# Kernel tuning notes

Measured on AMD Instinct MI355X. Metric: run time of the kernel, lower is better.

## Reference

```python
import jax, jax.numpy as jnp
import numpy as np

HEADS = 16
LN_EPS = 1e-5


def setup_inputs() -> dict:
    key = jax.random.key(0)
    ks = jax.random.split(key, 4)
    B, S, C, U = 2, 2048, 1024, 1024
    scale = 1.0 / np.sqrt(C)
    return {
        "inputs": jax.random.normal(ks[0], (B, S, C), dtype=jnp.float32),
        "Wq": jax.random.normal(ks[1], (C, U), dtype=jnp.float32) * scale,
        "bq": jnp.zeros((U,), dtype=jnp.float32),
        "Wk": jax.random.normal(ks[2], (C, U), dtype=jnp.float32) * scale,
        "bk": jnp.zeros((U,), dtype=jnp.float32),
        "Wv": jax.random.normal(ks[3], (C, U), dtype=jnp.float32) * scale,
        "bv": jnp.zeros((U,), dtype=jnp.float32),
        "ln_gamma": jnp.ones((S, U), dtype=jnp.float32),
        "ln_beta": jnp.zeros((S, U), dtype=jnp.float32),
    }


def reference(inputs, Wq, bq, Wk, bk, Wv, bv, ln_gamma, ln_beta):
    B, S, C = inputs.shape
    U = Wq.shape[1]
    H = HEADS
    dh = U // H

    Q = inputs @ Wq + bq  # [B,S,U]
    K = inputs @ Wk + bk
    V = inputs @ Wv + bv

    # torch: concat(split(X, U//H, dim=-1), dim=0) -> head-major stacking on batch
    def split_heads(X):
        return jnp.moveaxis(X.reshape(B, S, H, dh), 2, 0).reshape(H * B, S, dh)

    Q_, K_, V_ = split_heads(Q), split_heads(K), split_heads(V)

    scores = jnp.einsum('bqd,bkd->bqk', Q_, K_) / jnp.sqrt(jnp.float32(dh))
    tri = jnp.tril(jnp.ones((S, S), dtype=bool))  # causal mask
    scores = jnp.where(tri[None, :, :], scores, jnp.float32(-1e9))
    attn = jax.nn.softmax(scores, axis=-1)
    out_ = jnp.einsum('bqk,bkd->bqd', attn, V_)  # [H*B,S,dh]

    # inverse: split on batch into H chunks of size B, concat on feature dim
    out = jnp.moveaxis(out_.reshape(H, B, S, dh), 0, 2).reshape(B, S, U)

    out = out + inputs  # residual

    # LayerNorm over normalized_shape=[S, U] (joint seq+feature stats)
    mu = jnp.mean(out, axis=(-2, -1), keepdims=True)
    var = jnp.mean(jnp.square(out - mu), axis=(-2, -1), keepdims=True)
    out = (out - mu) / jnp.sqrt(var + LN_EPS) * ln_gamma + ln_beta
    return out
```

## Files before the change

kernel.cpp:

```cpp
#include <hip/hip_runtime.h>
#include <hip/hip_bf16.h>


typedef __bf16 bf16_t;
typedef __bf16 bf16x8 __attribute__((ext_vector_type(8)));
typedef __bf16 bf16x4 __attribute__((ext_vector_type(4)));
typedef _Float16 f16_t;
typedef _Float16 f16x2 __attribute__((ext_vector_type(2)));
typedef _Float16 f16x4 __attribute__((ext_vector_type(4)));
typedef _Float16 f16x8 __attribute__((ext_vector_type(8)));
typedef float f32x4 __attribute__((ext_vector_type(4)));

constexpr int Bsz = 2;
constexpr int Seq = 2048;
constexpr int Cdim = 1024;
constexpr int Udim = 1024;
constexpr int Hn = 16;
constexpr int Dh = 64;
constexpr int Mrows = Bsz * Seq;
constexpr int PerBatch = Seq * Udim;
constexpr float SCLQ = 0.125f * 1.44269504088896340736f;

#if __has_builtin(__builtin_amdgcn_exp2f)
#define EXP2F(x) __builtin_amdgcn_exp2f(x)
#else
#define EXP2F(x) exp2f(x)
#endif

#define AINL __attribute__((always_inline))
#define BARRIER() __builtin_amdgcn_s_barrier()
#define SCHEDB() __builtin_amdgcn_sched_barrier(0)
#define WAITV4() asm volatile("s_waitcnt vmcnt(4)" ::: "memory")
#define WAITV0() asm volatile("s_waitcnt vmcnt(0)" ::: "memory")

__device__ __forceinline__ void gload16(const void* g, void* l)
{
    __builtin_amdgcn_global_load_lds(
        (const __attribute__((address_space(1))) void*)g,
        (__attribute__((address_space(3))) void*)l, 16, 0, 0);
}

__device__ __forceinline__ f16x2 pkrtz(float a, float b)
{
    return __builtin_bit_cast(f16x2, __builtin_amdgcn_cvt_pkrtz(a, b));
}

__global__ __launch_bounds__(256)
void prep(const float* __restrict__ X,
          const float* __restrict__ Wq, const float* __restrict__ Wk,
          const float* __restrict__ Wv,
          bf16_t* __restrict__ Xb,
          bf16_t* __restrict__ Tq, bf16_t* __restrict__ Tk,
          bf16_t* __restrict__ Tv, float* __restrict__ stats)
{
    int z = blockIdx.z;
    int tid = threadIdx.x;
    if (z < 3) {
        const float* W = (z == 0) ? Wq : (z == 1) ? Wk : Wv;
        bf16_t* T = (z == 0) ? Tq : (z == 1) ? Tk : Tv;
        __shared__ bf16_t t[64][65];
        int x0 = blockIdx.x * 64, y0 = blockIdx.y * 64;
        int tx = tid & 63, ty = tid >> 6;
        for (int i = ty; i < 64; i += 4)
            t[i][tx] = (bf16_t)W[(size_t)(y0 + i) * Cdim + x0 + tx];
        __syncthreads();
        for (int i = ty; i < 64; i += 4)
            T[(size_t)(x0 + i) * Cdim + y0 + tx] = t[tx][i];
    } else {
        int bi = blockIdx.y * 16 + blockIdx.x;
        if (bi == 0 && tid < 4) stats[tid] = 0.0f;
        const float4* Xv = (const float4*)X;
#pragma unroll
        for (int k = 0; k < 16; k++) {
            int i = bi * 4096 + k * 256 + tid;
            float4 v = Xv[i];
            bf16x4 o = { (bf16_t)v.x, (bf16_t)v.y, (bf16_t)v.z, (bf16_t)v.w };
            *(bf16x4*)(Xb + (size_t)i * 4) = o;
        }
    }
}

__global__ __launch_bounds__(256)
void gemm_qkv(const bf16_t* __restrict__ X,
              const bf16_t* __restrict__ Wt0, const bf16_t* __restrict__ Wt1,
              const bf16_t* __restrict__ Wt2,
              const float* __restrict__ b0, const float* __restrict__ b1,
              const float* __restrict__ b2,
              f16_t* __restrict__ O0, f16_t* __restrict__ O1, f16_t* __restrict__ O2v)
{
    int z = blockIdx.z;
    const bf16_t* Wt = (z == 0) ? Wt0 : (z == 1) ? Wt1 : Wt2;
    const float* bias = (z == 0) ? b0 : (z == 1) ? b1 : b2;
    float scl = (z == 0) ? SCLQ : 1.0f;

    constexpr int Kd = 1024, Nd = 1024;
    __shared__ __align__(16) bf16_t As[2][4096];
    __shared__ __align__(16) bf16_t Bs[2][4096];

    int tid = threadIdx.x;
    int wave = tid >> 6, lane = tid & 63, quad = lane >> 4, l16 = lane & 15;
    int wm = (wave & 1) * 64, wn = (wave >> 1) * 64;
    int m0 = blockIdx.y * 128, n0 = blockIdx.x * 128;

    f32x4 acc[4][4] = {};

    int e0 = wave * 512 + lane * 8;
    int r0 = e0 >> 5, c0 = e0 & 31;
    int e1 = e0 + 2048;
    int r1 = e1 >> 5, c1 = e1 & 31;
    const bf16_t* Ag = X + (size_t)m0 * Kd;
    const bf16_t* Bg = Wt + (size_t)n0 * Kd;

    auto STG = [&](int nb, int k0) AINL {
        gload16(Ag + (size_t)r0 * Kd + k0 + c0, &As[nb][wave * 512]);
        gload16(Ag + (size_t)r1 * Kd + k0 + c1, &As[nb][2048 + wave * 512]);
        gload16(Bg + (size_t)r0 * Kd + k0 + c0, &Bs[nb][wave * 512]);
        gload16(Bg + (size_t)r1 * Kd + k0 + c1, &Bs[nb][2048 + wave * 512]);
    };

    int kNext = 32;
    auto STEP = [&](int buf, bool doStage) AINL {
        BARRIER();
        if (doStage) { STG(buf ^ 1, kNext); kNext += 32; WAITV4(); }
        else WAITV0();
        BARRIER();
        SCHEDB();
        bf16x8 af[4], bfr[4];
#pragma unroll
        for (int i = 0; i < 4; i++)
            af[i] = *(const bf16x8*)&As[buf][(wm + i * 16 + l16) * 32 + quad * 8];
#pragma unroll
        for (int i = 0; i < 4; i++)
            bfr[i] = *(const bf16x8*)&Bs[buf][(wn + i * 16 + l16) * 32 + quad * 8];
#pragma unroll
        for (int mt = 0; mt < 4; mt++)
#pragma unroll
            for (int nt = 0; nt < 4; nt++)
                acc[mt][nt] = __builtin_amdgcn_mfma_f32_16x16x32_bf16(
                    af[mt], bfr[nt], acc[mt][nt], 0, 0, 0);
    };

    STG(0, 0);
    for (int it = 0; it < 15; it++) { STEP(0, true); STEP(1, true); }
    STEP(0, true);
    STEP(1, false);

    if (z < 2) {
        f16_t* Og = (z == 0) ? O0 : O1;
#pragma unroll
        for (int nt = 0; nt < 4; nt++) {
            int col = n0 + wn + nt * 16 + l16;
            float bv = bias[col];
#pragma unroll
            for (int mt = 0; mt < 4; mt++) {
                int row = m0 + wm + mt * 16 + quad * 4;
#pragma unroll
                for (int r = 0; r < 4; r++)
                    Og[(size_t)(row + r) * Nd + col] = (f16_t)((acc[mt][nt][r] + bv) * scl);
            }
        }
    } else {
        int bb = m0 >> 11;
#pragma unroll
        for (int nt = 0; nt < 4; nt++) {
            int col = n0 + wn + nt * 16 + l16;
            float bv = bias[col];
            int h = col >> 6, d = col & 63;
            f16_t* vbase = O2v + (((size_t)(bb * Hn + h) * Dh + d) << 11);
#pragma unroll
            for (int mt = 0; mt < 4; mt++) {
                int row = m0 + wm + mt * 16 + quad * 4;
                int s = row & (Seq - 1);
                f16x4 pk;
#pragma unroll
                for (int r = 0; r < 4; r++) pk[r] = (f16_t)(acc[mt][nt][r] + bv);
                *(f16x4*)(vbase + s) = pk;
            }
        }
    }
}

__global__ __launch_bounds__(512, 4)
void attn15(const f16_t* __restrict__ Q, const f16_t* __restrict__ K,
            const f16_t* __restrict__ Vt, const float* __restrict__ X,
            bf16_t* __restrict__ R, float* __restrict__ stats)
{
    int id = blockIdx.x;
    int c = id & 7;
    int rr = id >> 3;
    int g = rr & 3;
    int pi = rr >> 2;
    int bh = (g << 3) | c;
    int b = bh >> 4, h = bh & 15;
    int qa = 31 - pi, qb = pi, split = 15 - pi;

    int tid = threadIdx.x;
    int grp = tid >> 8;
    int w = (tid >> 6) & 3;
    int lane = tid & 63, quad = lane >> 4, l16 = lane & 15;
    size_t bS = (size_t)b * Seq;

    __shared__ __align__(16) char ldsRaw[65600];
    f16_t* KsBase = (f16_t*)(ldsRaw + grp * 32768);
    f16_t* VsBase = (f16_t*)(ldsRaw + grp * 32768 + 16384);
    float* cmbO   = (float*)(ldsRaw + 32768);
    float* cmbLS  = (float*)(ldsRaw + 49152);
    float* red    = (float*)(ldsRaw + 65536);

    const f16_t* Kg = K + bS * Udim + h * Dh;
    const f16_t* Vg = Vt + ((size_t)(b * Hn + h)) * Dh * Seq;

    int srow = w * 8 + (lane >> 3);
    int schunk = (lane & 7) ^ ((lane >> 3) & 7);

    int qidxA = qa * 64 + w * 16 + l16;
    int qidxB = qb * 64 + w * 16 + l16;
    const f16_t* QpA = Q + (bS + qidxA) * Udim + h * Dh;
    const f16_t* QpB = Q + (bS + qidxB) * Udim + h * Dh;
    f16x8 qfA[2], qfB[2];
#pragma unroll
    for (int s2 = 0; s2 < 2; s2++) {
        qfA[s2] = *(const f16x8*)(QpA + s2 * 32 + quad * 8);
        qfB[s2] = *(const f16x8*)(QpB + s2 * 32 + quad * 8);
    }

    int m = l16 & 7;
    int kO0 = l16 * 64 + ((quad ^ m) << 3);
    int kO1 = l16 * 64 + (((4 + quad) ^ m) << 3);
    int vO[4];
#pragma unroll
    for (int t = 0; t < 4; t++)
        vO[t] = l16 * 64 + (((t * 32 + quad * 8) ^ (m << 4)) >> 1);

    f32x4 OA[4] = {}, OB[4] = {};
    float lsA = 0.0f, lsB = 0.0f;
    f32x4 stX[4], stY[4];

    auto tl0 = [&](int rho) AINL -> int { return (rho <= qb) ? rho : rho - qb - 1; };

    auto STAGE_K = [&](int nb, int tl) AINL {
        const f16_t* kp = Kg + (size_t)(tl * 64 + srow) * Udim + schunk * 8;
        f16_t* kd = KsBase + nb * 4096;
        gload16(kp, kd + w * 512);
        gload16(kp + (size_t)32 * Udim, kd + 2048 + w * 512);
    };
    auto STAGE_V = [&](int nb, int tl) AINL {
        const f16_t* vp = Vg + (size_t)srow * Seq + tl * 64 + schunk * 8;
        f16_t* vd = VsBase + nb * 4096;
        gload16(vp, vd + w * 512);
        gload16(vp + (size_t)32 * Seq, vd + 2048 + w * 512);
    };

    auto QK = [&](int buf, const f16x8 (&qf)[2], f32x4 (&sOUT)[4], int tcap) AINL {
        const f16_t* Kb = KsBase + buf * 4096;
#pragma unroll
        for (int t = 0; t < 4; t++) {
            if (t <= tcap) {
                f16x8 kf0 = *(const f16x8*)&Kb[kO0 + t * 1024];
                f16x8 kf1 = *(const f16x8*)&Kb[kO1 + t * 1024];
                f32x4 a = {};
                a = __builtin_amdgcn_mfma_f32_16x16x32_f16(kf0, qf[0], a, 0, 0, 0);
                a = __builtin_amdgcn_mfma_f32_16x16x32_f16(kf1, qf[1], a, 0, 0, 0);
                sOUT[t] = a;
            }
        }
    };

    auto SMPV = [&](f32x4 (&sIN)[4], f32x4 (&O)[4], float& ls, bool msk,
                    int kv0, int qidx, int tcap, int vbuf) AINL {
        const f16_t* Vb = VsBase + vbuf * 4096;
#pragma unroll
        for (int t = 0; t < 4; t++) {
            if (t <= tcap) {
                float pv[4];
#pragma unroll
                for (int r2 = 0; r2 < 4; r2++) {
                    float sv = sIN[t][r2];
                    if (msk && (kv0 + t * 16 + quad * 4 + r2 > qidx)) sv = -1e30f;
                    pv[r2] = EXP2F(sv);
                    ls += pv[r2];
                }
                f16x2 lo = pkrtz(pv[0], pv[1]);
                f16x2 hi = pkrtz(pv[2], pv[3]);
                f16x4 pf;
                pf[0] = lo[0]; pf[1] = lo[1]; pf[2] = hi[0]; pf[3] = hi[1];
#pragma unroll
                for (int dt = 0; dt < 4; dt++) {
                    f16x4 vf = *(const f16x4*)&Vb[vO[t] + dt * 1024];
                    O[dt] = __builtin_amdgcn_mfma_f32_16x16x16f16(vf, pf, O[dt], 0, 0, 0);
                }
            }
        }
    };

    auto ROUND = [&](int r, int buf, f32x4 (&sIN)[4], f32x4 (&sOUT)[4]) AINL {
        if (grp == 0) {
            if (r <= 14) STAGE_K(buf ^ 1, tl0(r + 1));
            if (r <= 15) STAGE_V(buf ^ 1, tl0(r));
        } else {
            if (r <= 15) STAGE_K(buf ^ 1, split + r + 1);
            STAGE_V(buf ^ 1, split + r);
        }
        if (grp == 0) {
            if (r <= 15) {
                if (r <= qb) QK(buf, qfB, sOUT, (r == qb) ? w : 3);
                else         QK(buf, qfA, sOUT, 3);
            }
        } else {
            QK(buf, qfA, sOUT, (r == 16) ? w : 3);
        }
        if (r >= 1) {
            if (grp == 0) {
                if (r <= qb)          SMPV(sIN, OB, lsB, false, 0, 0, 3, buf);
                else if (r == qb + 1) SMPV(sIN, OB, lsB, true, qb * 64, qidxB, w, buf);
                else                  SMPV(sIN, OA, lsA, false, 0, 0, 3, buf);
            } else {
                SMPV(sIN, OA, lsA, false, 0, 0, 3, buf);
            }
        }
        __syncthreads();
    };

    STAGE_K(0, (grp == 0) ? 0 : split);
    __syncthreads();

    for (int i = 0; i < 8; i++) {
        ROUND(2 * i, 0, stX, stY);
        ROUND(2 * i + 1, 1, stY, stX);
    }
    ROUND(16, 0, stX, stY);

    if (grp == 1)
        SMPV(stY, OA, lsA, true, qa * 64, qidxA, w, 1);

    __syncthreads();

    lsA += __shfl_xor(lsA, 16);
    lsA += __shfl_xor(lsA, 32);

    float s_acc = 0.0f, ss_acc = 0.0f;

    if (grp == 1) {
        float* po = cmbO + w * 1024 + lane * 16;
#pragma unroll
        for (int dt = 0; dt < 4; dt++)
            *(f32x4*)(po + dt * 4) = OA[dt];
        if (lane < 16) cmbLS[w * 16 + l16] = lsA;
    } else {
        lsB += __shfl_xor(lsB, 16);
        lsB += __shfl_xor(lsB, 32);
        float invB = 1.0f / lsB;
        const float* XpB = X + (bS + qidxB) * Udim + h * Dh;
        bf16_t* RpB = R + (bS + qidxB) * Udim + h * Dh;
#pragma unroll
        for (int dt = 0; dt < 4; dt++) {
            f32x4 xv = *(const f32x4*)(XpB + dt * 16 + quad * 4);
            f32x4 o = OB[dt] * invB + xv;
            bf16x4 ob;
#pragma unroll
            for (int r2 = 0; r2 < 4; r2++) {
                ob[r2] = (bf16_t)o[r2];
                s_acc += o[r2];
                ss_acc += o[r2] * o[r2];
            }
            *(bf16x4*)(RpB + dt * 16 + quad * 4) = ob;
        }
    }
    __syncthreads();

    if (grp == 0) {
        const float* po = cmbO + w * 1024 + lane * 16;
#pragma unroll
        for (int dt = 0; dt < 4; dt++)
            OA[dt] += *(const f32x4*)(po + dt * 4);
        lsA += cmbLS[w * 16 + l16];
        float invA = 1.0f / lsA;
        const float* XpA = X + (bS + qidxA) * Udim + h * Dh;
        bf16_t* RpA = R + (bS + qidxA) * Udim + h * Dh;
#pragma unroll
        for (int dt = 0; dt < 4; dt++) {
            f32x4 xv = *(const f32x4*)(XpA + dt * 16 + quad * 4);
            f32x4 o = OA[dt] * invA + xv;
            bf16x4 ob;
#pragma unroll
            for (int r2 = 0; r2 < 4; r2++) {
                ob[r2] = (bf16_t)o[r2];
                s_acc += o[r2];
                ss_acc += o[r2] * o[r2];
            }
            *(bf16x4*)(RpA + dt * 16 + quad * 4) = ob;
        }
    }

#pragma unroll
    for (int o = 1; o < 64; o <<= 1) {
        s_acc += __shfl_xor(s_acc, o);
        ss_acc += __shfl_xor(ss_acc, o);
    }
    int w8 = tid >> 6;
    if (lane == 0) { red[w8] = s_acc; red[8 + w8] = ss_acc; }
    __syncthreads();
    if (tid == 0) {
        float s = 0.0f, ss = 0.0f;
#pragma unroll
        for (int i = 0; i < 8; i++) { s += red[i]; ss += red[8 + i]; }
        atomicAdd(&stats[b], s);
        atomicAdd(&stats[2 + b], ss);
    }
}

__global__ __launch_bounds__(256)
void ln_norm(const bf16_t* __restrict__ R, const float* __restrict__ gamma,
             const float* __restrict__ beta, const float* __restrict__ stats,
             float* __restrict__ out)
{
    constexpr float invN = 1.0f / (float)PerBatch;
    float mu[2], inv[2];
#pragma unroll
    for (int b = 0; b < 2; b++) {
        float m = stats[b] * invN;
        float var = stats[2 + b] * invN - m * m;
        mu[b] = m;
        inv[b] = rsqrtf(var + 1e-5f);
    }
    int i = blockIdx.x * 256 + threadIdx.x;
    int f = i * 8;
    int b = f >> 21;
    int su = f & (PerBatch - 1);
    bf16x8 rv = *(const bf16x8*)(R + f);
    float4 g0 = *(const float4*)(gamma + su);
    float4 g1 = *(const float4*)(gamma + su + 4);
    float4 be0 = *(const float4*)(beta + su);
    float4 be1 = *(const float4*)(beta + su + 4);
    float4 o0, o1;
    o0.x = ((float)rv[0] - mu[b]) * inv[b] * g0.x + be0.x;
    o0.y = ((float)rv[1] - mu[b]) * inv[b] * g0.y + be0.y;
    o0.z = ((float)rv[2] - mu[b]) * inv[b] * g0.z + be0.z;
    o0.w = ((float)rv[3] - mu[b]) * inv[b] * g0.w + be0.w;
    o1.x = ((float)rv[4] - mu[b]) * inv[b] * g1.x + be1.x;
    o1.y = ((float)rv[5] - mu[b]) * inv[b] * g1.y + be1.y;
    o1.z = ((float)rv[6] - mu[b]) * inv[b] * g1.z + be1.z;
    o1.w = ((float)rv[7] - mu[b]) * inv[b] * g1.w + be1.w;
    *(float4*)(out + f) = o0;
    *(float4*)(out + f + 4) = o1;
}

extern "C" void kernel_launch(void* const* d_in, const int* in_sizes, int n_in,
                              void* d_out, int out_size, void* d_ws, size_t ws_size,
                              hipStream_t stream)
{
    const float* X     = (const float*)d_in[0];
    const float* Wq    = (const float*)d_in[1];
    const float* bq    = (const float*)d_in[2];
    const float* Wk    = (const float*)d_in[3];
    const float* bk    = (const float*)d_in[4];
    const float* Wv    = (const float*)d_in[5];
    const float* bv    = (const float*)d_in[6];
    const float* gamma = (const float*)d_in[7];
    const float* beta  = (const float*)d_in[8];
    float* out = (float*)d_out;

    char* ws = (char*)d_ws;
    size_t off = 0;
    auto alloc = [&](size_t bytes) -> void* {
        void* p = ws + off;
        off += (bytes + 255) & ~(size_t)255;
        return p;
    };
    bf16_t* Xb = (bf16_t*)alloc((size_t)Mrows * Cdim * 2);
    bf16_t* Tq = (bf16_t*)alloc((size_t)Cdim * Udim * 2);
    bf16_t* Tk = (bf16_t*)alloc((size_t)Cdim * Udim * 2);
    bf16_t* Tv = (bf16_t*)alloc((size_t)Cdim * Udim * 2);
    f16_t*  Qb = (f16_t*)alloc((size_t)Mrows * Udim * 2);
    f16_t*  Kb = (f16_t*)alloc((size_t)Mrows * Udim * 2);
    f16_t*  Vtb = (f16_t*)alloc((size_t)Mrows * Udim * 2);
    bf16_t* Rb = (bf16_t*)alloc((size_t)Mrows * Udim * 2);
    float*  stats = (float*)alloc(4 * sizeof(float));

    prep<<<dim3(16, 16, 4), 256, 0, stream>>>(X, Wq, Wk, Wv, Xb, Tq, Tk, Tv, stats);
    gemm_qkv<<<dim3(8, 32, 3), 256, 0, stream>>>(Xb, Tq, Tk, Tv, bq, bk, bv, Qb, Kb, Vtb);
    attn15<<<dim3(512), 512, 0, stream>>>(Qb, Kb, Vtb, X, Rb, stats);
    ln_norm<<<dim3(2048), 256, 0, stream>>>(Rb, gamma, beta, stats, out);
}
```

Baseline: 197.1 us.

## Restructure attention software pipeline to carry fp16 probabilities across rounds

Reorders the per-round attention pipeline. Each round now computes QK scores, runs PV on the previous round's probabilities (kept as packed fp16 fragments), then does the softmax exp for the current scores. This replaces carrying two fp32 score buffers between rounds. The V tile is staged into the current buffer so PV reads the previous one. The aim is to cut register pressure (fp16 instead of fp32 carry) and give MFMA and exp more room to overlap, at the cost of changed buffer indexing, which risks subtle races.

```diff
diff --git a/kernel.cpp b/kernel.cpp
--- a/kernel.cpp
+++ b/kernel.cpp
@@ -181,7 +181,7 @@
 }
 
 __global__ __launch_bounds__(512, 4)
-void attn15(const f16_t* __restrict__ Q, const f16_t* __restrict__ K,
+void attn16(const f16_t* __restrict__ Q, const f16_t* __restrict__ K,
             const f16_t* __restrict__ Vt, const float* __restrict__ X,
             bf16_t* __restrict__ R, float* __restrict__ stats)
 {
@@ -234,7 +234,7 @@
 
     f32x4 OA[4] = {}, OB[4] = {};
     float lsA = 0.0f, lsB = 0.0f;
-    f32x4 stX[4], stY[4];
+    f16x4 pfC[4] = {};
 
     auto tl0 = [&](int rho) AINL -> int { return (rho <= qb) ? rho : rho - qb - 1; };
 
@@ -251,7 +251,7 @@
         gload16(vp + (size_t)32 * Seq, vd + 2048 + w * 512);
     };
 
-    auto QK = [&](int buf, const f16x8 (&qf)[2], f32x4 (&sOUT)[4], int tcap) AINL {
+    auto QK = [&](int buf, const f16x8 (&qf)[2], f32x4 (&sc)[4], int tcap) AINL {
         const f16_t* Kb = KsBase + buf * 4096;
 #pragma unroll
         for (int t = 0; t < 4; t++) {
@@ -261,77 +261,94 @@
                 f32x4 a = {};
                 a = __builtin_amdgcn_mfma_f32_16x16x32_f16(kf0, qf[0], a, 0, 0, 0);
                 a = __builtin_amdgcn_mfma_f32_16x16x32_f16(kf1, qf[1], a, 0, 0, 0);
-                sOUT[t] = a;
-            }
-        }
-    };
-
-    auto SMPV = [&](f32x4 (&sIN)[4], f32x4 (&O)[4], float& ls, bool msk,
-                    int kv0, int qidx, int tcap, int vbuf) AINL {
-        const f16_t* Vb = VsBase + vbuf * 4096;
+                sc[t] = a;
+            }
+        }
+    };
+
+    auto PV = [&](int vb, f32x4 (&O)[4], int ptc) AINL {
+        const f16_t* Vb = VsBase + vb * 4096;
+#pragma unroll
+        for (int t = 0; t < 4; t++) {
+            if (t <= ptc) {
+#pragma unroll
+                for (int dt = 0; dt < 4; dt++) {
+                    f16x4 vf = *(const f16x4*)&Vb[vO[t] + dt * 1024];
+                    O[dt] = __builtin_amdgcn_mfma_f32_16x16x16f16(vf, pfC[t], O[dt], 0, 0, 0);
+                }
+            }
+        }
+    };
+
+    auto SM = [&](f32x4 (&sc)[4], float& ls, bool msk, int kv0, int qidx, int tcap) AINL {
 #pragma unroll
         for (int t = 0; t < 4; t++) {
             if (t <= tcap) {
                 float pv[4];
 #pragma unroll
                 for (int r2 = 0; r2 < 4; r2++) {
-                    float sv = sIN[t][r2];
+                    float sv = sc[t][r2];
                     if (msk && (kv0 + t * 16 + quad * 4 + r2 > qidx)) sv = -1e30f;
                     pv[r2] = EXP2F(sv);
                     ls += pv[r2];
                 }
                 f16x2 lo = pkrtz(pv[0], pv[1]);
                 f16x2 hi = pkrtz(pv[2], pv[3]);
-                f16x4 pf;
-                pf[0] = lo[0]; pf[1] = lo[1]; pf[2] = hi[0]; pf[3] = hi[1];
-#pragma unroll
-                for (int dt = 0; dt < 4; dt++) {
-                    f16x4 vf = *(const f16x4*)&Vb[vO[t] + dt * 1024];
-                    O[dt] = __builtin_amdgcn_mfma_f32_16x16x16f16(vf, pf, O[dt], 0, 0, 0);
-                }
-            }
-        }
-    };
-
-    auto ROUND = [&](int r, int buf, f32x4 (&sIN)[4], f32x4 (&sOUT)[4]) AINL {
+                pfC[t][0] = lo[0]; pfC[t][1] = lo[1];
+                pfC[t][2] = hi[0]; pfC[t][3] = hi[1];
+            }
+        }
+    };
+
+    int r = 0;
+    auto ROUND = [&](int buf) AINL {
         if (grp == 0) {
             if (r <= 14) STAGE_K(buf ^ 1, tl0(r + 1));
-            if (r <= 15) STAGE_V(buf ^ 1, tl0(r));
+            if (r <= 15) STAGE_V(buf, tl0(r));
         } else {
             if (r <= 15) STAGE_K(buf ^ 1, split + r + 1);
-            STAGE_V(buf ^ 1, split + r);
-        }
-        if (grp == 0) {
-            if (r <= 15) {
-                if (r <= qb) QK(buf, qfB, sOUT, (r == qb) ? w : 3);
-                else         QK(buf, qfA, sOUT, 3);
-            }
-        } else {
-            QK(buf, qfA, sOUT, (r == 16) ? w : 3);
+            STAGE_V(buf, split + r);
+        }
+        f32x4 sc[4];
+        bool doQK = (grp == 1) || (r <= 15);
+        if (doQK) {
+            if (grp == 0) {
+                if (r <= qb) QK(buf, qfB, sc, (r == qb) ? w : 3);
+                else         QK(buf, qfA, sc, 3);
+            } else {
+                QK(buf, qfA, sc, (r == 16) ? w : 3);
+            }
         }
         if (r >= 1) {
             if (grp == 0) {
-                if (r <= qb)          SMPV(sIN, OB, lsB, false, 0, 0, 3, buf);
-                else if (r == qb + 1) SMPV(sIN, OB, lsB, true, qb * 64, qidxB, w, buf);
-                else                  SMPV(sIN, OA, lsA, false, 0, 0, 3, buf);
+                if (r - 1 <= qb) PV(buf ^ 1, OB, (r - 1 == qb) ? w : 3);
+                else             PV(buf ^ 1, OA, 3);
             } else {
-                SMPV(sIN, OA, lsA, false, 0, 0, 3, buf);
+                PV(buf ^ 1, OA, 3);
+            }
+        }
+        if (doQK) {
+            if (grp == 0) {
+                if (r < qb)       SM(sc, lsB, false, 0, 0, 3);
+                else if (r == qb) SM(sc, lsB, true, qb * 64, qidxB, w);
+                else              SM(sc, lsA, false, 0, 0, 3);
+            } else {
+                if (r == 16) SM(sc, lsA, true, qa * 64, qidxA, w);
+                else         SM(sc, lsA, false, 0, 0, 3);
             }
         }
         __syncthreads();
+        r++;
     };
 
     STAGE_K(0, (grp == 0) ? 0 : split);
     __syncthreads();
 
-    for (int i = 0; i < 8; i++) {
-        ROUND(2 * i, 0, stX, stY);
-        ROUND(2 * i + 1, 1, stY, stX);
-    }
-    ROUND(16, 0, stX, stY);
+    for (int i = 0; i < 8; i++) { ROUND(0); ROUND(1); }
+    ROUND(0);
 
     if (grp == 1)
-        SMPV(stY, OA, lsA, true, qa * 64, qidxA, w, 1);
+        PV(0, OA, w);
 
     __syncthreads();
 
@@ -479,6 +496,6 @@
 
     prep<<<dim3(16, 16, 4), 256, 0, stream>>>(X, Wq, Wk, Wv, Xb, Tq, Tk, Tv, stats);
     gemm_qkv<<<dim3(8, 32, 3), 256, 0, stream>>>(Xb, Tq, Tk, Tv, bq, bk, bv, Qb, Kb, Vtb);
-    attn15<<<dim3(512), 512, 0, stream>>>(Qb, Kb, Vtb, X, Rb, stats);
+    attn16<<<dim3(512), 512, 0, stream>>>(Qb, Kb, Vtb, X, Rb, stats);
     ln_norm<<<dim3(2048), 256, 0, stream>>>(Rb, gamma, beta, stats, out);
 }
```

Result: faster. 183.5 us (-6.9%).
